# Optimization experiments

Hardware: AMD Instinct MI355X
Metric: run time of the kernel (lower is better)

The kernel has to match this reference:

```python
import jax, jax.numpy as jnp
import numpy as np

IN_F = 4096
OUT_F = 4096
B, S = 4, 2048


def _quantize_weight(w_float):
    """Replicates Int4PackedLinear.__init__ double quantization; returns reg_b and w_scale."""
    w_amax = jnp.abs(w_float).max()
    scale = jnp.where(w_amax == 0, 1.0, w_amax / 127.0)
    w_int8 = jnp.clip(jnp.round(w_float / scale), -127, 127).astype(jnp.int8)
    low4_amax = jnp.abs(w_int8.astype(jnp.float32)).max()
    low4_scale = jnp.where(low4_amax == 0, 1.0, low4_amax / 7.0)
    w_low = jnp.clip(jnp.round(w_int8.astype(jnp.float32) / low4_scale), -7, 7).astype(jnp.int8)
    w_rec = jnp.round(w_low.astype(jnp.float32) * low4_scale).astype(jnp.int8)
    w_high = jnp.clip(w_int8.astype(jnp.int32) - w_rec.astype(jnp.int32), -7, 7).astype(jnp.int8)
    reg_b = (w_rec.astype(jnp.int32) + w_high.astype(jnp.int32)).astype(jnp.int8)  # w_combined
    return reg_b, scale.astype(jnp.float32)


def setup_inputs() -> dict:
    key = jax.random.key(0)
    k1, k2, k3 = jax.random.split(key, 3)
    w_float = jax.random.normal(k1, (OUT_F, IN_F), dtype=jnp.float32) * 0.02
    reg_b, w_scale = _quantize_weight(w_float)
    x = jax.random.normal(k2, (B, S, IN_F), dtype=jnp.float32)
    bias = jax.random.normal(k3, (OUT_F,), dtype=jnp.float32) * 0.01
    # gate=1.0 >= threshold=0.3 -> full-precision INT8 path uses reg_b
    return {"x": x, "w_int": reg_b, "w_scale": w_scale, "bias": bias}


def reference(x, w_int, w_scale, bias):
    # --- dynamic per-tensor activation quantization ---
    x_amax = jnp.abs(x).max()
    x_scale = jnp.where(x_amax == 0, jnp.float32(1.0), x_amax / 127.0)
    x_int8 = jnp.clip(jnp.round(x / x_scale), -127, 127).astype(jnp.int8)
    # --- integer matmul (accumulate in int32, like torch._int_mm) ---
    out_i32 = jnp.einsum(
        'bsk,nk->bsn',
        x_int8.astype(jnp.int32),
        w_int.astype(jnp.int32),
    )  # [B, S, OUT_F]
    # --- dequant scale in bf16 AFTER the integer matmul, then bias add ---
    combined_scale = (x_scale * w_scale).astype(jnp.bfloat16)
    out = out_i32.astype(jnp.bfloat16) * combined_scale
    out = out + bias  # bf16 + fp32 -> fp32, matching torch promotion
    return out
```

## Files before the change

### kernel.cpp

```cpp
#include <hip/hip_runtime.h>
#include <hip/hip_bf16.h>
#include <stdint.h>

#define IN_F  4096
#define OUT_F 4096
#define BSZ   4
#define SEQ   2048
#define MDIM  (BSZ * SEQ)

typedef __attribute__((address_space(1))) uint8_t ga_u8_t;
typedef __attribute__((address_space(3))) uint8_t ls_u8_t;

__device__ __forceinline__ void gload16_lds(const void* g, void* l) {
    __builtin_amdgcn_global_load_lds((ga_u8_t*)g, (ls_u8_t*)l, 16, 0, 0);
}

__device__ __forceinline__ float bf16_rne(float f) {
    unsigned u = __float_as_uint(f);
    u = (u + 0x7fffu + ((u >> 16) & 1u)) & 0xffff0000u;
    return __uint_as_float(u);
}

__global__ void amax_kernel(const float* __restrict__ x, int n4,
                            unsigned int* __restrict__ amax_u) {
    const float4* x4 = (const float4*)x;
    int idx = blockIdx.x * blockDim.x + threadIdx.x;
    int stride = gridDim.x * blockDim.x;
    float m = 0.0f;
    for (int i = idx; i < n4; i += stride) {
        float4 v = x4[i];
        m = fmaxf(m, fmaxf(fmaxf(fabsf(v.x), fabsf(v.y)),
                           fmaxf(fabsf(v.z), fabsf(v.w))));
    }
    for (int off = 32; off > 0; off >>= 1)
        m = fmaxf(m, __shfl_down(m, off, 64));
    __shared__ float sm[4];
    int lane = threadIdx.x & 63, wave = threadIdx.x >> 6;
    if (lane == 0) sm[wave] = m;
    __syncthreads();
    if (threadIdx.x == 0) {
        m = fmaxf(fmaxf(sm[0], sm[1]), fmaxf(sm[2], sm[3]));
        atomicMax(amax_u, __float_as_uint(m));
    }
}

__global__ void prep_kernel(const float* __restrict__ x,
                            const int* __restrict__ w,
                            signed char* __restrict__ x8,
                            signed char* __restrict__ w8,
                            const unsigned int* __restrict__ amax_u,
                            int nx4, int nw4) {
    int idx = blockIdx.x * blockDim.x + threadIdx.x;
    if (idx < nx4) {
        float amax = __uint_as_float(*amax_u);
        float xs = (amax == 0.0f) ? 1.0f : (amax / 127.0f);
        float4 v = ((const float4*)x)[idx];
        char4 q;
        q.x = (signed char)fminf(fmaxf(rintf(v.x / xs), -127.0f), 127.0f);
        q.y = (signed char)fminf(fmaxf(rintf(v.y / xs), -127.0f), 127.0f);
        q.z = (signed char)fminf(fmaxf(rintf(v.z / xs), -127.0f), 127.0f);
        q.w = (signed char)fminf(fmaxf(rintf(v.w / xs), -127.0f), 127.0f);
        ((char4*)x8)[idx] = q;
    } else {
        int widx = idx - nx4;
        if (widx < nw4) {
            int4 v = ((const int4*)w)[widx];
            char4 q;
            q.x = (signed char)v.x; q.y = (signed char)v.y;
            q.z = (signed char)v.z; q.w = (signed char)v.w;
            ((char4*)w8)[widx] = q;
        }
    }
}

using i32x4 = __attribute__((ext_vector_type(4))) int;

#define FENCE() asm volatile("" ::: "memory")
#define BAR()   do { FENCE(); __builtin_amdgcn_s_barrier(); FENCE(); } while (0)
#define WAITV4() asm volatile("s_waitcnt vmcnt(4)" ::: "memory")
#define WAITV0() asm volatile("s_waitcnt vmcnt(0)" ::: "memory")
#define WAITL0() asm volatile("s_waitcnt lgkmcnt(0)" ::: "memory")

#define MFMA8(P)                                                             \
    _Pragma("unroll")                                                        \
    for (int j = 0; j < 4; ++j) {                                            \
        acc[2*(P)][j]   = __builtin_amdgcn_mfma_i32_16x16x64_i8(             \
            aX, bF[j], acc[2*(P)][j], 0, 0, 0);                              \
        acc[2*(P)+1][j] = __builtin_amdgcn_mfma_i32_16x16x64_i8(             \
            aY, bF[j], acc[2*(P)+1][j], 0, 0, 0);                            \
    }

#define PHASE_TAIL(P)                                                        \
    BAR();                                                                   \
    WAITL0();                                                                \
    __builtin_amdgcn_sched_barrier(0);                                       \
    __builtin_amdgcn_s_setprio(1);                                           \
    MFMA8(P);                                                                \
    __builtin_amdgcn_s_setprio(0);                                           \
    BAR();

#define TILE(T, DOSTAGE, TW3)                                                \
    {                                                                        \
        const signed char* base = smem + ((T) % 3) * 32768;                  \
        signed char* sbase = smem + (((T) + 2) % 3) * 32768;                 \
        const int kst = ((T) + 2) * 64;                                      \
                                      \
        bF[0] = *(const i32x4*)(base + boff[0]);                             \
        bF[1] = *(const i32x4*)(base + boff[1]);                             \
        bF[2] = *(const i32x4*)(base + boff[2]);                             \
        bF[3] = *(const i32x4*)(base + boff[3]);                             \
        aX = *(const i32x4*)(base + aoff[0]);                                \
        aY = *(const i32x4*)(base + aoff[1]);                                \
        if (DOSTAGE) gload16_lds(gA0 + kst, sbase + dA0);                    \
        PHASE_TAIL(0)                                                        \
                                                                \
        aX = *(const i32x4*)(base + aoff[2]);                                \
        aY = *(const i32x4*)(base + aoff[3]);                                \
        if (DOSTAGE) gload16_lds(gA1 + kst, sbase + dA1);                    \
        PHASE_TAIL(1)                                                        \
                                                                \
        aX = *(const i32x4*)(base + aoff[4]);                                \
        aY = *(const i32x4*)(base + aoff[5]);                                \
        if (DOSTAGE) gload16_lds(gB0 + kst, sbase + dB0);                    \
        PHASE_TAIL(2)                                                        \
                                                                \
        aX = *(const i32x4*)(base + aoff[6]);                                \
        aY = *(const i32x4*)(base + aoff[7]);                                \
        if (DOSTAGE) gload16_lds(gB1 + kst, sbase + dB1);                    \
        TW3;                                                                 \
        PHASE_TAIL(3)                                                        \
    }

__global__ __launch_bounds__(512, 2) void gemm_i8_kernel(
    const signed char* __restrict__ A,
    const signed char* __restrict__ B,
    const unsigned int* __restrict__ amax_u,
    const float* __restrict__ wscale_p,
    const float* __restrict__ bias,
    float* __restrict__ out) {
    __shared__ signed char smem[3 * 32768];

    const int tid = threadIdx.x;
    const int lane = tid & 63;
    const int wave = tid >> 6;
    const int wm = wave >> 2;
    const int wn = wave & 3;

    const int bid = blockIdx.x;
    const int wg = (bid & 7) * 64 + (bid >> 3);
    const int mt = wg >> 4;
    const int nt = wg & 15;
    const int tileM = mt * 256;
    const int tileN = nt * 256;

    const int g = tid;
    const int srow = g >> 2;
    const int scol = ((g & 3) ^ ((srow >> 1) & 3)) * 16;
    const signed char* gA0 = A + (size_t)(tileM +       srow) * IN_F + scol;
    const signed char* gA1 = A + (size_t)(tileM + 128 + srow) * IN_F + scol;
    const signed char* gB0 = B + (size_t)(tileN +       srow) * IN_F + scol;
    const signed char* gB1 = B + (size_t)(tileN + 128 + srow) * IN_F + scol;
    const int dA0 = g * 16;
    const int dA1 = 8192  + g * 16;
    const int dB0 = 16384 + g * 16;
    const int dB1 = 24576 + g * 16;

    int aoff[8], boff[4];
    const int kc = lane >> 4;
#pragma unroll
    for (int i = 0; i < 8; ++i) {
        int r = wm * 128 + i * 16 + (lane & 15);
        aoff[i] = r * 64 + ((kc ^ ((r >> 1) & 3)) * 16);
    }
#pragma unroll
    for (int j = 0; j < 4; ++j) {
        int r = wn * 64 + j * 16 + (lane & 15);
        boff[j] = 16384 + r * 64 + ((kc ^ ((r >> 1) & 3)) * 16);
    }

    i32x4 acc[8][4] = {};
    i32x4 bF[4], aX, aY;

    gload16_lds(gA0,      smem + dA0);
    gload16_lds(gA1,      smem + dA1);
    gload16_lds(gB0,      smem + dB0);
    gload16_lds(gB1,      smem + dB1);
    gload16_lds(gA0 + 64, smem + 32768 + dA0);
    gload16_lds(gA1 + 64, smem + 32768 + dA1);
    gload16_lds(gB0 + 64, smem + 32768 + dB0);
    gload16_lds(gB1 + 64, smem + 32768 + dB1);
    WAITV4();
    BAR();

    for (int kt = 0; kt < 62; ++kt) {
        TILE(kt, true, WAITV4());
    }
    TILE(62, false, WAITV0());
    TILE(63, false, (void)0);

    float amax = __uint_as_float(*amax_u);
    float xs = (amax == 0.0f) ? 1.0f : (amax / 127.0f);
    float cs = bf16_rne(xs * wscale_p[0]);

#pragma unroll
    for (int j = 0; j < 4; ++j) {
        int n = tileN + wn * 64 + j * 16 + (lane & 15);
        float bz = bias[n];
#pragma unroll
        for (int i = 0; i < 8; ++i) {
            int row0 = tileM + wm * 128 + i * 16 + (lane >> 4) * 4;
#pragma unroll
            for (int r = 0; r < 4; ++r) {
                float v = bf16_rne((float)acc[i][j][r]);
                float p = bf16_rne(v * cs);
                __builtin_nontemporal_store(
                    p + bz, &out[(size_t)(row0 + r) * OUT_F + n]);
            }
        }
    }
}

extern "C" void kernel_launch(void* const* d_in, const int* in_sizes, int n_in,
                              void* d_out, int out_size, void* d_ws,
                              size_t ws_size, hipStream_t stream) {
    const float* x = (const float*)d_in[0];
    const int* w_int = (const int*)d_in[1];
    const float* w_scale = (const float*)d_in[2];
    const float* bias = (const float*)d_in[3];
    float* out = (float*)d_out;

    unsigned char* ws = (unsigned char*)d_ws;
    unsigned int* amax_u = (unsigned int*)ws;
    signed char* w8 = (signed char*)(ws + 64);
    signed char* x8 = (signed char*)(ws + 64 + (size_t)OUT_F * IN_F);

    hipMemsetAsync(amax_u, 0, 4, stream);

    const int n_x4 = MDIM * IN_F / 4;
    const int n_w4 = OUT_F * IN_F / 4;

    amax_kernel<<<4096, 256, 0, stream>>>(x, n_x4, amax_u);
    prep_kernel<<<(n_x4 + n_w4) / 256, 256, 0, stream>>>(
        x, w_int, x8, w8, amax_u, n_x4, n_w4);

    const int nblocks = (MDIM / 256) * (OUT_F / 256);
    gemm_i8_kernel<<<nblocks, 512, 0, stream>>>(x8, w8, amax_u, w_scale, bias,
                                                out);
}
```

Before: 427.4 us.

## Software-pipeline LDS fragment reads with double-buffered registers across k-tiles

Restructures the int8 MFMA main loop so LDS fragment loads for the next phase and the next k-tile's B and A fragments are issued before the current phase's MFMAs. It uses ping-pong register sets and partial lgkmcnt waits instead of a full wait before each phase. The goal is to hide LDS read latency behind MFMA execution. In exchange it needs more registers, which at 2 waves/SIMD with a 128-entry accumulator may cause spills, and it relies on fragile hand-tuned waitcnt counts.

```diff
diff --git a/kernel.cpp b/kernel.cpp
--- a/kernel.cpp
+++ b/kernel.cpp
@@ -77,59 +77,62 @@
 
 #define FENCE() asm volatile("" ::: "memory")
 #define BAR()   do { FENCE(); __builtin_amdgcn_s_barrier(); FENCE(); } while (0)
-#define WAITV4() asm volatile("s_waitcnt vmcnt(4)" ::: "memory")
-#define WAITV0() asm volatile("s_waitcnt vmcnt(0)" ::: "memory")
-#define WAITL0() asm volatile("s_waitcnt lgkmcnt(0)" ::: "memory")
-
-#define MFMA8(P)                                                             \
+#define WAITV(N) asm volatile("s_waitcnt vmcnt(" #N ")" ::: "memory")
+#define WAITL(N) asm volatile("s_waitcnt lgkmcnt(" #N ")" ::: "memory")
+#define SB()    __builtin_amdgcn_sched_barrier(0)
+#define PRIO1() __builtin_amdgcn_s_setprio(1)
+#define PRIO0() __builtin_amdgcn_s_setprio(0)
+
+#define MFMA_PH(P, X, Y, BF)                                                 \
     _Pragma("unroll")                                                        \
     for (int j = 0; j < 4; ++j) {                                            \
         acc[2*(P)][j]   = __builtin_amdgcn_mfma_i32_16x16x64_i8(             \
-            aX, bF[j], acc[2*(P)][j], 0, 0, 0);                              \
+            X, BF[j], acc[2*(P)][j], 0, 0, 0);                               \
         acc[2*(P)+1][j] = __builtin_amdgcn_mfma_i32_16x16x64_i8(             \
-            aY, bF[j], acc[2*(P)+1][j], 0, 0, 0);                            \
-    }
-
-#define PHASE_TAIL(P)                                                        \
+            Y, BF[j], acc[2*(P)+1][j], 0, 0, 0);                             \
+    }
+
+#define TILE_P(T, BFc, BFn, DOSTAGE, DOPREF, WVC2, WL2, WL3)                 \
+  {                                                                          \
+    const signed char* base  = smem + ((T) % 3) * 32768;                     \
+    const signed char* nbase = smem + (((T) + 1) % 3) * 32768;               \
+    signed char* sbase = smem + (((T) + 2) % 3) * 32768;                     \
+    const int kst = ((T) + 2) * 64;                                          \
+                         \
+    q0 = *(const i32x4*)(base + aoff[2]);                                    \
+    q1 = *(const i32x4*)(base + aoff[3]);                                    \
+    if (DOSTAGE) gload16_lds(gA0 + kst, sbase + dA0);                        \
+    BAR(); WAITL(2); SB(); PRIO1();                                          \
+    MFMA_PH(0, p0, p1, BFc); PRIO0(); BAR();                                 \
+                                    \
+    p0 = *(const i32x4*)(base + aoff[4]);                                    \
+    p1 = *(const i32x4*)(base + aoff[5]);                                    \
+    if (DOSTAGE) gload16_lds(gA1 + kst, sbase + dA1);                        \
+    BAR(); WAITL(2); SB(); PRIO1();                                          \
+    MFMA_PH(1, q0, q1, BFc); PRIO0(); BAR();                                 \
+                                \
+    q0 = *(const i32x4*)(base + aoff[6]);                                    \
+    q1 = *(const i32x4*)(base + aoff[7]);                                    \
+    if (DOSTAGE) gload16_lds(gB0 + kst, sbase + dB0);                        \
+    WVC2;                                                                    \
     BAR();                                                                   \
-    WAITL0();                                                                \
-    __builtin_amdgcn_sched_barrier(0);                                       \
-    __builtin_amdgcn_s_setprio(1);                                           \
-    MFMA8(P);                                                                \
-    __builtin_amdgcn_s_setprio(0);                                           \
-    BAR();
-
-#define TILE(T, DOSTAGE, TW3)                                                \
-    {                                                                        \
-        const signed char* base = smem + ((T) % 3) * 32768;                  \
-        signed char* sbase = smem + (((T) + 2) % 3) * 32768;                 \
-        const int kst = ((T) + 2) * 64;                                      \
-                                      \
-        bF[0] = *(const i32x4*)(base + boff[0]);                             \
-        bF[1] = *(const i32x4*)(base + boff[1]);                             \
-        bF[2] = *(const i32x4*)(base + boff[2]);                             \
-        bF[3] = *(const i32x4*)(base + boff[3]);                             \
-        aX = *(const i32x4*)(base + aoff[0]);                                \
-        aY = *(const i32x4*)(base + aoff[1]);                                \
-        if (DOSTAGE) gload16_lds(gA0 + kst, sbase + dA0);                    \
-        PHASE_TAIL(0)                                                        \
-                                                                \
-        aX = *(const i32x4*)(base + aoff[2]);                                \
-        aY = *(const i32x4*)(base + aoff[3]);                                \
-        if (DOSTAGE) gload16_lds(gA1 + kst, sbase + dA1);                    \
-        PHASE_TAIL(1)                                                        \
-                                                                \
-        aX = *(const i32x4*)(base + aoff[4]);                                \
-        aY = *(const i32x4*)(base + aoff[5]);                                \
-        if (DOSTAGE) gload16_lds(gB0 + kst, sbase + dB0);                    \
-        PHASE_TAIL(2)                                                        \
-                                                                \
-        aX = *(const i32x4*)(base + aoff[6]);                                \
-        aY = *(const i32x4*)(base + aoff[7]);                                \
-        if (DOSTAGE) gload16_lds(gB1 + kst, sbase + dB1);                    \
-        TW3;                                                                 \
-        PHASE_TAIL(3)                                                        \
-    }
+    if (DOPREF) {                                                            \
+        BFn[0] = *(const i32x4*)(nbase + boff[0]);                           \
+        BFn[1] = *(const i32x4*)(nbase + boff[1]);                           \
+    }                                                                        \
+    WL2; SB(); PRIO1();                                                      \
+    MFMA_PH(2, p0, p1, BFc); PRIO0(); BAR();                                 \
+         \
+    if (DOPREF) {                                                            \
+        BFn[2] = *(const i32x4*)(nbase + boff[2]);                           \
+        BFn[3] = *(const i32x4*)(nbase + boff[3]);                           \
+        p0 = *(const i32x4*)(nbase + aoff[0]);                               \
+        p1 = *(const i32x4*)(nbase + aoff[1]);                               \
+    }                                                                        \
+    if (DOSTAGE) gload16_lds(gB1 + kst, sbase + dB1);                        \
+    BAR(); WL3; SB(); PRIO1();                                               \
+    MFMA_PH(3, q0, q1, BFc); PRIO0(); BAR();                                 \
+  }
 
 __global__ __launch_bounds__(512, 2) void gemm_i8_kernel(
     const signed char* __restrict__ A,
@@ -179,7 +182,8 @@
     }
 
     i32x4 acc[8][4] = {};
-    i32x4 bF[4], aX, aY;
+    i32x4 bA[4], bB[4];
+    i32x4 p0, p1, q0, q1;
 
     gload16_lds(gA0,      smem + dA0);
     gload16_lds(gA1,      smem + dA1);
@@ -189,14 +193,21 @@
     gload16_lds(gA1 + 64, smem + 32768 + dA1);
     gload16_lds(gB0 + 64, smem + 32768 + dB0);
     gload16_lds(gB1 + 64, smem + 32768 + dB1);
-    WAITV4();
+    WAITV(4);
     BAR();
-
-    for (int kt = 0; kt < 62; ++kt) {
-        TILE(kt, true, WAITV4());
-    }
-    TILE(62, false, WAITV0());
-    TILE(63, false, (void)0);
+    bA[0] = *(const i32x4*)(smem + boff[0]);
+    bA[1] = *(const i32x4*)(smem + boff[1]);
+    bA[2] = *(const i32x4*)(smem + boff[2]);
+    bA[3] = *(const i32x4*)(smem + boff[3]);
+    p0 = *(const i32x4*)(smem + aoff[0]);
+    p1 = *(const i32x4*)(smem + aoff[1]);
+
+    for (int kt = 0; kt < 62; kt += 2) {
+        TILE_P(kt,     bA, bB, 1, 1, WAITV(3), WAITL(4), WAITL(6));
+        TILE_P(kt + 1, bB, bA, 1, 1, WAITV(3), WAITL(4), WAITL(6));
+    }
+    TILE_P(62, bA, bB, 0, 1, WAITV(0), WAITL(4), WAITL(6));
+    TILE_P(63, bB, bA, 0, 0, (void)0,  WAITL(2), WAITL(0));
 
     float amax = __uint_as_float(*amax_u);
     float xs = (amax == 0.0f) ? 1.0f : (amax / 127.0f);
```

Measured after the change: 424.9 us. Within noise of the previous version (-0.6%).

## Collapse four-phase barrier pipeline into one barrier per K-tile with unrolled buffers

Applied to the files above, without the earlier changes.

The main K loop now does one barrier per 64-wide K tile instead of eight. After that barrier it issues all four async global-to-LDS loads for the tile two steps ahead, loads all A and B fragments from LDS, then runs all 32 MFMAs. The loop is unrolled by three so the triple-buffer indices are compile-time constants, and the s_setprio and sched_barrier hints are dropped. This cuts barrier and scheduling overhead, at the cost of more live fragment registers and leaving the compiler to interleave LDS reads with MFMAs.

```diff
diff --git a/kernel.cpp b/kernel.cpp
--- a/kernel.cpp
+++ b/kernel.cpp
@@ -77,59 +77,32 @@
 
 #define FENCE() asm volatile("" ::: "memory")
 #define BAR()   do { FENCE(); __builtin_amdgcn_s_barrier(); FENCE(); } while (0)
-#define WAITV4() asm volatile("s_waitcnt vmcnt(4)" ::: "memory")
-#define WAITV0() asm volatile("s_waitcnt vmcnt(0)" ::: "memory")
-#define WAITL0() asm volatile("s_waitcnt lgkmcnt(0)" ::: "memory")
-
-#define MFMA8(P)                                                             \
+#define WAITV(N) asm volatile("s_waitcnt vmcnt(" #N ")" ::: "memory")
+
+#define TILE1(BUF, SBUF, KST, DOSTAGE, WV)                                   \
+  {                                                                          \
+    const signed char* base = smem + (BUF) * 32768;                          \
+    BAR();                                                                   \
+    if (DOSTAGE) {                                                           \
+        signed char* sb = smem + (SBUF) * 32768;                             \
+        gload16_lds(gA0 + (KST), sb + dA0);                                  \
+        gload16_lds(gA1 + (KST), sb + dA1);                                  \
+        gload16_lds(gB0 + (KST), sb + dB0);                                  \
+        gload16_lds(gB1 + (KST), sb + dB1);                                  \
+    }                                                                        \
+    WV;                                                                      \
+    i32x4 bF[4], aF[8];                                                      \
     _Pragma("unroll")                                                        \
-    for (int j = 0; j < 4; ++j) {                                            \
-        acc[2*(P)][j]   = __builtin_amdgcn_mfma_i32_16x16x64_i8(             \
-            aX, bF[j], acc[2*(P)][j], 0, 0, 0);                              \
-        acc[2*(P)+1][j] = __builtin_amdgcn_mfma_i32_16x16x64_i8(             \
-            aY, bF[j], acc[2*(P)+1][j], 0, 0, 0);                            \
-    }
-
-#define PHASE_TAIL(P)                                                        \
-    BAR();                                                                   \
-    WAITL0();                                                                \
-    __builtin_amdgcn_sched_barrier(0);                                       \
-    __builtin_amdgcn_s_setprio(1);                                           \
-    MFMA8(P);                                                                \
-    __builtin_amdgcn_s_setprio(0);                                           \
-    BAR();
-
-#define TILE(T, DOSTAGE, TW3)                                                \
-    {                                                                        \
-        const signed char* base = smem + ((T) % 3) * 32768;                  \
-        signed char* sbase = smem + (((T) + 2) % 3) * 32768;                 \
-        const int kst = ((T) + 2) * 64;                                      \
-                                      \
-        bF[0] = *(const i32x4*)(base + boff[0]);                             \
-        bF[1] = *(const i32x4*)(base + boff[1]);                             \
-        bF[2] = *(const i32x4*)(base + boff[2]);                             \
-        bF[3] = *(const i32x4*)(base + boff[3]);                             \
-        aX = *(const i32x4*)(base + aoff[0]);                                \
-        aY = *(const i32x4*)(base + aoff[1]);                                \
-        if (DOSTAGE) gload16_lds(gA0 + kst, sbase + dA0);                    \
-        PHASE_TAIL(0)                                                        \
-                                                                \
-        aX = *(const i32x4*)(base + aoff[2]);                                \
-        aY = *(const i32x4*)(base + aoff[3]);                                \
-        if (DOSTAGE) gload16_lds(gA1 + kst, sbase + dA1);                    \
-        PHASE_TAIL(1)                                                        \
-                                                                \
-        aX = *(const i32x4*)(base + aoff[4]);                                \
-        aY = *(const i32x4*)(base + aoff[5]);                                \
-        if (DOSTAGE) gload16_lds(gB0 + kst, sbase + dB0);                    \
-        PHASE_TAIL(2)                                                        \
-                                                                \
-        aX = *(const i32x4*)(base + aoff[6]);                                \
-        aY = *(const i32x4*)(base + aoff[7]);                                \
-        if (DOSTAGE) gload16_lds(gB1 + kst, sbase + dB1);                    \
-        TW3;                                                                 \
-        PHASE_TAIL(3)                                                        \
-    }
+    for (int j = 0; j < 4; ++j) bF[j] = *(const i32x4*)(base + boff[j]);     \
+    _Pragma("unroll")                                                        \
+    for (int i = 0; i < 8; ++i) aF[i] = *(const i32x4*)(base + aoff[i]);     \
+    _Pragma("unroll")                                                        \
+    for (int i = 0; i < 8; ++i)                                              \
+      _Pragma("unroll")                                                      \
+      for (int j = 0; j < 4; ++j)                                            \
+        acc[i][j] = __builtin_amdgcn_mfma_i32_16x16x64_i8(                   \
+            aF[i], bF[j], acc[i][j], 0, 0, 0);                               \
+  }
 
 __global__ __launch_bounds__(512, 2) void gemm_i8_kernel(
     const signed char* __restrict__ A,
@@ -179,7 +152,6 @@
     }
 
     i32x4 acc[8][4] = {};
-    i32x4 bF[4], aX, aY;
 
     gload16_lds(gA0,      smem + dA0);
     gload16_lds(gA1,      smem + dA1);
@@ -189,14 +161,17 @@
     gload16_lds(gA1 + 64, smem + 32768 + dA1);
     gload16_lds(gB0 + 64, smem + 32768 + dB0);
     gload16_lds(gB1 + 64, smem + 32768 + dB1);
-    WAITV4();
-    BAR();
-
-    for (int kt = 0; kt < 62; ++kt) {
-        TILE(kt, true, WAITV4());
-    }
-    TILE(62, false, WAITV0());
-    TILE(63, false, (void)0);
+    WAITV(4);
+
+    for (int kt = 0; kt < 60; kt += 3) {
+        TILE1(0, 2, (kt + 2) * 64, 1, WAITV(4));
+        TILE1(1, 0, (kt + 3) * 64, 1, WAITV(4));
+        TILE1(2, 1, (kt + 4) * 64, 1, WAITV(4));
+    }
+    TILE1(0, 2, 62 * 64, 1, WAITV(4));
+    TILE1(1, 0, 63 * 64, 1, WAITV(4));
+    TILE1(2, 0, 0,       0, WAITV(0));
+    TILE1(0, 0, 0,       0, (void)0);
 
     float amax = __uint_as_float(*amax_u);
     float xs = (amax == 0.0f) ? 1.0f : (amax / 127.0f);
```

New measurement: 433.2 us. No clear change (+1.4%).
